# Kernel optimization log

Hardware: AMD Instinct MI355X
Metric: run time of the kernel (lower is better)

## Reference

```python
import jax, jax.numpy as jnp
import numpy as np

BN_EPS = 1e-5


def lstm_scan(x, Wih, Whh, b):
    # x: [B, T, I] -> outputs [B, T, H]; PyTorch gate order i, f, g, o
    B = x.shape[0]
    H = Whh.shape[1]
    xs = jnp.swapaxes(x, 0, 1)  # [T, B, I]

    def step(carry, xt):
        h, c = carry
        z = xt @ Wih.T + h @ Whh.T + b  # [B, 4H]
        i, f, g, o = jnp.split(z, 4, axis=-1)
        c = jax.nn.sigmoid(f) * c + jax.nn.sigmoid(i) * jnp.tanh(g)
        h = jax.nn.sigmoid(o) * jnp.tanh(c)
        return (h, c), h

    init = (jnp.zeros((B, H), x.dtype), jnp.zeros((B, H), x.dtype))
    _, hs = jax.lax.scan(step, init, xs)
    return jnp.swapaxes(hs, 0, 1)


def bilstm(x, Wf, Uf, bf, Wr, Ur, br):
    fwd = lstm_scan(x, Wf, Uf, bf)
    rev = lstm_scan(x[:, ::-1], Wr, Ur, br)[:, ::-1]
    return jnp.concatenate([fwd, rev], axis=-1)


def batchnorm(x, g, b):
    # training-mode BN: batch mean, biased variance (PyTorch forward default)
    mu = x.mean(axis=0)
    var = x.var(axis=0)
    return g * (x - mu) * jax.lax.rsqrt(var + BN_EPS) + b


def setup_inputs() -> dict:
    key = jax.random.key(0)
    ks = jax.random.split(key, 20)
    B = 1048576
    idx = jax.random.randint(ks[0], (B, 1), 0, 8).astype(jnp.float32)
    feats = jax.random.normal(ks[1], (B, 7), dtype=jnp.float32)
    x = jnp.concatenate([idx, feats], axis=1)  # [B, 8]

    def p(k, shape):
        return 0.1 * jax.random.normal(k, shape, dtype=jnp.float32)

    return {
        "x": x,
        "emb": p(ks[2], (8, 2)),
        "W1": p(ks[3], (18, 9)), "b1": p(ks[4], (18,)),
        "g1": jnp.ones((18,), jnp.float32), "be1": jnp.zeros((18,), jnp.float32),
        "W2": p(ks[5], (9, 18)), "b2": p(ks[6], (9,)),
        "g2": jnp.ones((9,), jnp.float32), "be2": jnp.zeros((9,), jnp.float32),
        # lstm1: input 1, hidden 2, bidirectional
        "l1Wf": p(ks[7], (8, 1)), "l1Uf": p(ks[8], (8, 2)), "l1bf": p(ks[9], (8,)),
        "l1Wr": p(ks[10], (8, 1)), "l1Ur": p(ks[11], (8, 2)), "l1br": p(ks[12], (8,)),
        # lstm2: input 4, hidden 1, bidirectional
        "l2Wf": p(ks[13], (4, 4)), "l2Uf": p(ks[14], (4, 1)), "l2bf": p(ks[15], (4,)),
        "l2Wr": p(ks[16], (4, 4)), "l2Ur": p(ks[17], (4, 1)), "l2br": p(ks[18], (4,)),
    }


def reference(x, emb, W1, b1, g1, be1, W2, b2, g2, be2,
              l1Wf, l1Uf, l1bf, l1Wr, l1Ur, l1br,
              l2Wf, l2Uf, l2bf, l2Wr, l2Ur, l2br):
    idx = x[:, 0].astype(jnp.int32)
    e = emb[idx]                                   # [B, 2]
    h = jnp.concatenate([e, x[:, 1:]], axis=1)     # [B, 9]
    h = jax.nn.relu(batchnorm(h @ W1.T + b1, g1, be1))   # [B, 18]
    h = jax.nn.relu(batchnorm(h @ W2.T + b2, g2, be2))   # [B, 9]
    h = h[:, :, None]                              # [B, 9, 1]
    h = jax.nn.relu(bilstm(h, l1Wf, l1Uf, l1bf, l1Wr, l1Ur, l1br))  # [B, 9, 4]
    h = bilstm(h, l2Wf, l2Uf, l2bf, l2Wr, l2Ur, l2br)               # [B, 9, 2]
    return h.reshape(-1, 9, 2)
```

## Files before the change

kernel.cpp:

```cpp
#include <hip/hip_runtime.h>

#define LOG2E 1.4426950408889634f
#define BN_EPS 1e-5f

__device__ __forceinline__ float sigf(float x){
    return __builtin_amdgcn_rcpf(1.f + __builtin_amdgcn_exp2f(-LOG2E * x));
}
__device__ __forceinline__ float tanh_(float x){
    return 1.f - 2.f * __builtin_amdgcn_rcpf(__builtin_amdgcn_exp2f((2.f*LOG2E) * x) + 1.f);
}
__device__ __forceinline__ float relu_(float x){ return fmaxf(x, 0.f); }

__device__ __forceinline__ float wsum(float v){
    #pragma unroll
    for (int m = 32; m >= 1; m >>= 1) v += __shfl_xor(v, m, 64);
    return v;
}

__device__ __forceinline__ void z1_row(const float* __restrict__ x, const float* __restrict__ emb,
                                       const float* __restrict__ W1, const float* __restrict__ b1,
                                       long row, float z1[18])
{
    const float4* xv = (const float4*)(x + row * 8);
    float4 p = xv[0];
    float4 q = xv[1];
    int idx = (int)p.x;
    float2 e = ((const float2*)emb)[idx];
    float h0[9];
    h0[0] = e.x; h0[1] = e.y;
    h0[2] = p.y; h0[3] = p.z; h0[4] = p.w;
    h0[5] = q.x; h0[6] = q.y; h0[7] = q.z; h0[8] = q.w;
    #pragma unroll
    for (int k = 0; k < 18; ++k){
        float s = b1[k];
        #pragma unroll
        for (int j = 0; j < 9; ++j) s = fmaf(W1[k*9 + j], h0[j], s);
        z1[k] = s;
    }
}

__global__ __launch_bounds__(256) void k_stats1(const float* __restrict__ x, const float* __restrict__ emb,
                                                const float* __restrict__ W1, const float* __restrict__ b1,
                                                float* __restrict__ stats, int B)
{
    float as[18], aq[18];
    #pragma unroll
    for (int k = 0; k < 18; ++k){ as[k] = 0.f; aq[k] = 0.f; }
    long base = (long)blockIdx.x * 1024 + threadIdx.x;
    #pragma unroll
    for (int r = 0; r < 4; ++r){
        long row = base + r * 256;
        if (row < B){
            float z1[18];
            z1_row(x, emb, W1, b1, row, z1);
            #pragma unroll
            for (int k = 0; k < 18; ++k){ as[k] += z1[k]; aq[k] = fmaf(z1[k], z1[k], aq[k]); }
        }
    }
    __shared__ float sm[36];
    if (threadIdx.x < 36) sm[threadIdx.x] = 0.f;
    __syncthreads();
    bool l0 = (threadIdx.x & 63) == 0;
    #pragma unroll
    for (int k = 0; k < 18; ++k){
        float s = wsum(as[k]);
        float q = wsum(aq[k]);
        if (l0){ atomicAdd(&sm[k], s); atomicAdd(&sm[18 + k], q); }
    }
    __syncthreads();
    if (threadIdx.x < 36) atomicAdd(&stats[threadIdx.x], sm[threadIdx.x]);
}

__global__ __launch_bounds__(256) void k_stats2(const float* __restrict__ x, const float* __restrict__ emb,
                                                const float* __restrict__ W1, const float* __restrict__ b1,
                                                const float* __restrict__ g1, const float* __restrict__ be1,
                                                const float* __restrict__ W2, const float* __restrict__ b2,
                                                float* __restrict__ stats, int B)
{
    float invB = 1.f / (float)B;
    float sc[18], sh[18];
    #pragma unroll
    for (int k = 0; k < 18; ++k){
        float mu  = stats[k] * invB;
        float var = fmaf(-mu, mu, stats[18 + k] * invB);
        float rs  = __builtin_amdgcn_rsqf(var + BN_EPS);
        sc[k] = g1[k] * rs;
        sh[k] = fmaf(-mu, sc[k], be1[k]);
    }
    float as[9], aq[9];
    #pragma unroll
    for (int k = 0; k < 9; ++k){ as[k] = 0.f; aq[k] = 0.f; }
    long base = (long)blockIdx.x * 1024 + threadIdx.x;
    #pragma unroll
    for (int r = 0; r < 4; ++r){
        long row = base + r * 256;
        if (row < B){
            float z1[18];
            z1_row(x, emb, W1, b1, row, z1);
            float a1[18];
            #pragma unroll
            for (int k = 0; k < 18; ++k) a1[k] = relu_(fmaf(sc[k], z1[k], sh[k]));
            #pragma unroll
            for (int k = 0; k < 9; ++k){
                float s = b2[k];
                #pragma unroll
                for (int j = 0; j < 18; ++j) s = fmaf(W2[k*18 + j], a1[j], s);
                as[k] += s; aq[k] = fmaf(s, s, aq[k]);
            }
        }
    }
    __shared__ float sm[18];
    if (threadIdx.x < 18) sm[threadIdx.x] = 0.f;
    __syncthreads();
    bool l0 = (threadIdx.x & 63) == 0;
    #pragma unroll
    for (int k = 0; k < 9; ++k){
        float s = wsum(as[k]);
        float q = wsum(aq[k]);
        if (l0){ atomicAdd(&sm[k], s); atomicAdd(&sm[9 + k], q); }
    }
    __syncthreads();
    if (threadIdx.x < 18) atomicAdd(&stats[36 + threadIdx.x], sm[threadIdx.x]);
}

template<bool REV>
__device__ __forceinline__ void lstm1(const float* __restrict__ W, const float* __restrict__ U,
                                      const float* __restrict__ bb, const float xin[9], float out[9][2])
{
    float h[2] = {0.f, 0.f}, c[2] = {0.f, 0.f};
    #pragma unroll
    for (int s = 0; s < 9; ++s){
        const int t = REV ? 8 - s : s;
        float xt = xin[t];
        float z[8];
        #pragma unroll
        for (int r = 0; r < 8; ++r)
            z[r] = fmaf(W[r], xt, fmaf(U[2*r], h[0], fmaf(U[2*r + 1], h[1], bb[r])));
        #pragma unroll
        for (int k = 0; k < 2; ++k){
            float ig = sigf(z[k]);
            float fg = sigf(z[2 + k]);
            float gg = tanh_(z[4 + k]);
            float og = sigf(z[6 + k]);
            c[k] = fmaf(fg, c[k], ig * gg);
            h[k] = og * tanh_(c[k]);
        }
        out[t][0] = h[0]; out[t][1] = h[1];
    }
}

template<bool REV>
__device__ __forceinline__ void lstm2(const float* __restrict__ W, const float* __restrict__ U,
                                      const float* __restrict__ bb, const float uin[9][4], float out[9])
{
    float h = 0.f, c = 0.f;
    #pragma unroll
    for (int s = 0; s < 9; ++s){
        const int t = REV ? 8 - s : s;
        float z[4];
        #pragma unroll
        for (int r = 0; r < 4; ++r){
            float acc = fmaf(U[r], h, bb[r]);
            #pragma unroll
            for (int j = 0; j < 4; ++j) acc = fmaf(W[4*r + j], uin[t][j], acc);
            z[r] = acc;
        }
        float ig = sigf(z[0]);
        float fg = sigf(z[1]);
        float gg = tanh_(z[2]);
        float og = sigf(z[3]);
        c = fmaf(fg, c, ig * gg);
        h = og * tanh_(c);
        out[t] = h;
    }
}

__global__ __launch_bounds__(256) void k_main(const float* __restrict__ x, const float* __restrict__ emb,
    const float* __restrict__ W1, const float* __restrict__ b1,
    const float* __restrict__ g1, const float* __restrict__ be1,
    const float* __restrict__ W2, const float* __restrict__ b2,
    const float* __restrict__ g2, const float* __restrict__ be2,
    const float* __restrict__ w1f, const float* __restrict__ u1f, const float* __restrict__ c1f,
    const float* __restrict__ w1r, const float* __restrict__ u1r, const float* __restrict__ c1r,
    const float* __restrict__ w2f, const float* __restrict__ u2f, const float* __restrict__ c2f,
    const float* __restrict__ w2r, const float* __restrict__ u2r, const float* __restrict__ c2r,
    const float* __restrict__ stats, float* __restrict__ out, int B)
{
    long row = (long)blockIdx.x * 256 + threadIdx.x;
    if (row >= B) return;
    float invB = 1.f / (float)B;

    float z1[18];
    z1_row(x, emb, W1, b1, row, z1);
    float a1[18];
    #pragma unroll
    for (int k = 0; k < 18; ++k){
        float mu  = stats[k] * invB;
        float var = fmaf(-mu, mu, stats[18 + k] * invB);
        float rs  = __builtin_amdgcn_rsqf(var + BN_EPS);
        a1[k] = relu_(fmaf(g1[k] * rs, z1[k] - mu, be1[k]));
    }
    float a2[9];
    #pragma unroll
    for (int k = 0; k < 9; ++k){
        float s = b2[k];
        #pragma unroll
        for (int j = 0; j < 18; ++j) s = fmaf(W2[k*18 + j], a1[j], s);
        float mu  = stats[36 + k] * invB;
        float var = fmaf(-mu, mu, stats[45 + k] * invB);
        float rs  = __builtin_amdgcn_rsqf(var + BN_EPS);
        a2[k] = relu_(fmaf(g2[k] * rs, s - mu, be2[k]));
    }

    float hf[9][2], hr[9][2];
    lstm1<false>(w1f, u1f, c1f, a2, hf);
    lstm1<true >(w1r, u1r, c1r, a2, hr);

    float u[9][4];
    #pragma unroll
    for (int t = 0; t < 9; ++t){
        u[t][0] = relu_(hf[t][0]);
        u[t][1] = relu_(hf[t][1]);
        u[t][2] = relu_(hr[t][0]);
        u[t][3] = relu_(hr[t][1]);
    }

    float of[9], orr[9];
    lstm2<false>(w2f, u2f, c2f, u, of);
    lstm2<true >(w2r, u2r, c2r, u, orr);

    float2* op = (float2*)(out + row * 18);
    #pragma unroll
    for (int t = 0; t < 9; ++t) op[t] = make_float2(of[t], orr[t]);
}

extern "C" void kernel_launch(void* const* d_in, const int* in_sizes, int n_in,
                              void* d_out, int out_size, void* d_ws, size_t ws_size,
                              hipStream_t stream)
{
    const float* x    = (const float*)d_in[0];
    const float* emb  = (const float*)d_in[1];
    const float* W1   = (const float*)d_in[2];
    const float* b1   = (const float*)d_in[3];
    const float* g1   = (const float*)d_in[4];
    const float* be1  = (const float*)d_in[5];
    const float* W2   = (const float*)d_in[6];
    const float* b2   = (const float*)d_in[7];
    const float* g2   = (const float*)d_in[8];
    const float* be2  = (const float*)d_in[9];
    const float* l1Wf = (const float*)d_in[10];
    const float* l1Uf = (const float*)d_in[11];
    const float* l1bf = (const float*)d_in[12];
    const float* l1Wr = (const float*)d_in[13];
    const float* l1Ur = (const float*)d_in[14];
    const float* l1br = (const float*)d_in[15];
    const float* l2Wf = (const float*)d_in[16];
    const float* l2Uf = (const float*)d_in[17];
    const float* l2bf = (const float*)d_in[18];
    const float* l2Wr = (const float*)d_in[19];
    const float* l2Ur = (const float*)d_in[20];
    const float* l2br = (const float*)d_in[21];

    int B = in_sizes[0] / 8;
    float* stats = (float*)d_ws;

    hipMemsetAsync(d_ws, 0, 64 * sizeof(float), stream);

    int nb12 = (B + 1023) / 1024;
    int nb3  = (B + 255) / 256;

    k_stats1<<<nb12, 256, 0, stream>>>(x, emb, W1, b1, stats, B);
    k_stats2<<<nb12, 256, 0, stream>>>(x, emb, W1, b1, g1, be1, W2, b2, stats, B);
    k_main<<<nb3, 256, 0, stream>>>(x, emb, W1, b1, g1, be1, W2, b2, g2, be2,
                                    l1Wf, l1Uf, l1bf, l1Wr, l1Ur, l1br,
                                    l2Wf, l2Uf, l2bf, l2Wr, l2Ur, l2br,
                                    stats, (float*)d_out, B);
}
```

Before: 163.1 us.

## Compute BN1 stats from input moments, cache z2, vectorize fused LSTM gates

The first stats pass now accumulates first and second moments of the 9-wide input, and the layer-1 BN mean and variance are derived from these with W1 per block. This removes the 18-wide matmul from that pass. When the workspace is large enough, the second stats pass stores the pre-BN layer-2 activations so the main kernel skips recomputing layer 1 and 2 and reads 36 B/row instead. The forward and reverse LSTM directions run together in packed float vectors, and sigmoid*tanh is fused into a single reciprocal. The risks are the extra global write and read traffic for z2 and some numerical drift in the moment-based variance.

```diff
diff --git a/kernel.cpp b/kernel.cpp
--- a/kernel.cpp
+++ b/kernel.cpp
@@ -3,11 +3,18 @@
 #define LOG2E 1.4426950408889634f
 #define BN_EPS 1e-5f
 
+typedef float f32x2 __attribute__((ext_vector_type(2)));
+typedef float f32x4 __attribute__((ext_vector_type(4)));
+
 __device__ __forceinline__ float sigf(float x){
     return __builtin_amdgcn_rcpf(1.f + __builtin_amdgcn_exp2f(-LOG2E * x));
 }
-__device__ __forceinline__ float tanh_(float x){
-    return 1.f - 2.f * __builtin_amdgcn_rcpf(__builtin_amdgcn_exp2f((2.f*LOG2E) * x) + 1.f);
+__device__ __forceinline__ float sigtanh(float a, float b){
+    float A  = __builtin_amdgcn_exp2f(LOG2E * a);
+    float Bv = __builtin_amdgcn_exp2f((2.f * LOG2E) * b);
+    float num = A * (Bv - 1.f);
+    float den = (1.f + A) * (1.f + Bv);
+    return num * __builtin_amdgcn_rcpf(den);
 }
 __device__ __forceinline__ float relu_(float x){ return fmaxf(x, 0.f); }
 
@@ -17,95 +24,134 @@
     return v;
 }
 
-__device__ __forceinline__ void z1_row(const float* __restrict__ x, const float* __restrict__ emb,
-                                       const float* __restrict__ W1, const float* __restrict__ b1,
-                                       long row, float z1[18])
+__device__ constexpr int TRI(int j, int l){ return j*9 - j*(j-1)/2 + (l - j); }
+
+__device__ __forceinline__ void load_h0(const float* __restrict__ x, const float* __restrict__ emb,
+                                        long row, float h0[9])
 {
     const float4* xv = (const float4*)(x + row * 8);
     float4 p = xv[0];
     float4 q = xv[1];
     int idx = (int)p.x;
     float2 e = ((const float2*)emb)[idx];
-    float h0[9];
     h0[0] = e.x; h0[1] = e.y;
     h0[2] = p.y; h0[3] = p.z; h0[4] = p.w;
     h0[5] = q.x; h0[6] = q.y; h0[7] = q.z; h0[8] = q.w;
-    #pragma unroll
-    for (int k = 0; k < 18; ++k){
-        float s = b1[k];
-        #pragma unroll
-        for (int j = 0; j < 9; ++j) s = fmaf(W1[k*9 + j], h0[j], s);
-        z1[k] = s;
-    }
-}
-
-__global__ __launch_bounds__(256) void k_stats1(const float* __restrict__ x, const float* __restrict__ emb,
-                                                const float* __restrict__ W1, const float* __restrict__ b1,
-                                                float* __restrict__ stats, int B)
-{
-    float as[18], aq[18];
-    #pragma unroll
-    for (int k = 0; k < 18; ++k){ as[k] = 0.f; aq[k] = 0.f; }
+}
+
+__global__ __launch_bounds__(256) void k_moments(const float* __restrict__ x, const float* __restrict__ emb,
+                                                 float* __restrict__ stats, int B)
+{
+    float s9[9], mt[45];
+    #pragma unroll
+    for (int j = 0; j < 9; ++j) s9[j] = 0.f;
+    #pragma unroll
+    for (int t = 0; t < 45; ++t) mt[t] = 0.f;
+
     long base = (long)blockIdx.x * 1024 + threadIdx.x;
     #pragma unroll
     for (int r = 0; r < 4; ++r){
         long row = base + r * 256;
         if (row < B){
-            float z1[18];
-            z1_row(x, emb, W1, b1, row, z1);
-            #pragma unroll
-            for (int k = 0; k < 18; ++k){ as[k] += z1[k]; aq[k] = fmaf(z1[k], z1[k], aq[k]); }
-        }
-    }
-    __shared__ float sm[36];
-    if (threadIdx.x < 36) sm[threadIdx.x] = 0.f;
+            float h0[9];
+            load_h0(x, emb, row, h0);
+            #pragma unroll
+            for (int j = 0; j < 9; ++j){
+                s9[j] += h0[j];
+                #pragma unroll
+                for (int l = j; l < 9; ++l)
+                    mt[TRI(j,l)] = fmaf(h0[j], h0[l], mt[TRI(j,l)]);
+            }
+        }
+    }
+    __shared__ float sm[54];
+    if (threadIdx.x < 54) sm[threadIdx.x] = 0.f;
     __syncthreads();
     bool l0 = (threadIdx.x & 63) == 0;
     #pragma unroll
-    for (int k = 0; k < 18; ++k){
-        float s = wsum(as[k]);
-        float q = wsum(aq[k]);
-        if (l0){ atomicAdd(&sm[k], s); atomicAdd(&sm[18 + k], q); }
-    }
-    __syncthreads();
-    if (threadIdx.x < 36) atomicAdd(&stats[threadIdx.x], sm[threadIdx.x]);
-}
-
+    for (int j = 0; j < 9; ++j){
+        float v = wsum(s9[j]);
+        if (l0) atomicAdd(&sm[j], v);
+    }
+    #pragma unroll
+    for (int t = 0; t < 45; ++t){
+        float v = wsum(mt[t]);
+        if (l0) atomicAdd(&sm[9 + t], v);
+    }
+    __syncthreads();
+    if (threadIdx.x < 9)  atomicAdd(&stats[threadIdx.x], sm[threadIdx.x]);
+    else if (threadIdx.x < 54) atomicAdd(&stats[16 + threadIdx.x - 9], sm[threadIdx.x]);
+}
+
+__device__ __forceinline__ void bn1_from_moments(const float* __restrict__ stats,
+                                                 const float* __restrict__ W1, const float* __restrict__ b1,
+                                                 const float* __restrict__ g1, const float* __restrict__ be1,
+                                                 float invB, float* smem_sc, float* smem_sh)
+{
+    if (threadIdx.x < 18){
+        int k = threadIdx.x;
+        float w[9];
+        #pragma unroll
+        for (int j = 0; j < 9; ++j) w[j] = W1[k*9 + j];
+        float dot9 = 0.f, q = 0.f;
+        #pragma unroll
+        for (int j = 0; j < 9; ++j){
+            dot9 = fmaf(w[j], stats[j], dot9);
+            q = fmaf(w[j]*w[j], stats[16 + TRI(j,j)], q);
+            #pragma unroll
+            for (int l = j+1; l < 9; ++l)
+                q = fmaf(2.f*w[j]*w[l], stats[16 + TRI(j,l)], q);
+        }
+        float m1  = dot9 * invB;
+        float var = fmaf(-m1, m1, q * invB);
+        float mu  = m1 + b1[k];
+        float sc  = g1[k] * __builtin_amdgcn_rsqf(var + BN_EPS);
+        smem_sc[k] = sc;
+        smem_sh[k] = fmaf(-mu, sc, be1[k]);
+    }
+    __syncthreads();
+}
+
+template<int STORE_Z2>
 __global__ __launch_bounds__(256) void k_stats2(const float* __restrict__ x, const float* __restrict__ emb,
                                                 const float* __restrict__ W1, const float* __restrict__ b1,
                                                 const float* __restrict__ g1, const float* __restrict__ be1,
                                                 const float* __restrict__ W2, const float* __restrict__ b2,
-                                                float* __restrict__ stats, int B)
-{
-    float invB = 1.f / (float)B;
-    float sc[18], sh[18];
-    #pragma unroll
-    for (int k = 0; k < 18; ++k){
-        float mu  = stats[k] * invB;
-        float var = fmaf(-mu, mu, stats[18 + k] * invB);
-        float rs  = __builtin_amdgcn_rsqf(var + BN_EPS);
-        sc[k] = g1[k] * rs;
-        sh[k] = fmaf(-mu, sc[k], be1[k]);
-    }
+                                                float* __restrict__ stats, float* __restrict__ z2buf, int B)
+{
+    __shared__ float s_sc[18], s_sh[18];
+    bn1_from_moments(stats, W1, b1, g1, be1, 1.f/(float)B, s_sc, s_sh);
+
+    float sc1[18], sh1[18];
+    #pragma unroll
+    for (int k = 0; k < 18; ++k){ sc1[k] = s_sc[k]; sh1[k] = s_sh[k]; }
+
     float as[9], aq[9];
     #pragma unroll
     for (int k = 0; k < 9; ++k){ as[k] = 0.f; aq[k] = 0.f; }
+
     long base = (long)blockIdx.x * 1024 + threadIdx.x;
     #pragma unroll
     for (int r = 0; r < 4; ++r){
         long row = base + r * 256;
         if (row < B){
-            float z1[18];
-            z1_row(x, emb, W1, b1, row, z1);
+            float h0[9];
+            load_h0(x, emb, row, h0);
             float a1[18];
             #pragma unroll
-            for (int k = 0; k < 18; ++k) a1[k] = relu_(fmaf(sc[k], z1[k], sh[k]));
+            for (int k = 0; k < 18; ++k){
+                float s = b1[k];
+                #pragma unroll
+                for (int j = 0; j < 9; ++j) s = fmaf(W1[k*9 + j], h0[j], s);
+                a1[k] = relu_(fmaf(sc1[k], s, sh1[k]));
+            }
             #pragma unroll
             for (int k = 0; k < 9; ++k){
                 float s = b2[k];
                 #pragma unroll
                 for (int j = 0; j < 18; ++j) s = fmaf(W2[k*18 + j], a1[j], s);
                 as[k] += s; aq[k] = fmaf(s, s, aq[k]);
+                if (STORE_Z2) z2buf[(long)k * B + row] = s;
             }
         }
     }
@@ -120,61 +166,14 @@
         if (l0){ atomicAdd(&sm[k], s); atomicAdd(&sm[9 + k], q); }
     }
     __syncthreads();
-    if (threadIdx.x < 18) atomicAdd(&stats[36 + threadIdx.x], sm[threadIdx.x]);
-}
-
-template<bool REV>
-__device__ __forceinline__ void lstm1(const float* __restrict__ W, const float* __restrict__ U,
-                                      const float* __restrict__ bb, const float xin[9], float out[9][2])
-{
-    float h[2] = {0.f, 0.f}, c[2] = {0.f, 0.f};
-    #pragma unroll
-    for (int s = 0; s < 9; ++s){
-        const int t = REV ? 8 - s : s;
-        float xt = xin[t];
-        float z[8];
-        #pragma unroll
-        for (int r = 0; r < 8; ++r)
-            z[r] = fmaf(W[r], xt, fmaf(U[2*r], h[0], fmaf(U[2*r + 1], h[1], bb[r])));
-        #pragma unroll
-        for (int k = 0; k < 2; ++k){
-            float ig = sigf(z[k]);
-            float fg = sigf(z[2 + k]);
-            float gg = tanh_(z[4 + k]);
-            float og = sigf(z[6 + k]);
-            c[k] = fmaf(fg, c[k], ig * gg);
-            h[k] = og * tanh_(c[k]);
-        }
-        out[t][0] = h[0]; out[t][1] = h[1];
-    }
-}
-
-template<bool REV>
-__device__ __forceinline__ void lstm2(const float* __restrict__ W, const float* __restrict__ U,
-                                      const float* __restrict__ bb, const float uin[9][4], float out[9])
-{
-    float h = 0.f, c = 0.f;
-    #pragma unroll
-    for (int s = 0; s < 9; ++s){
-        const int t = REV ? 8 - s : s;
-        float z[4];
-        #pragma unroll
-        for (int r = 0; r < 4; ++r){
-            float acc = fmaf(U[r], h, bb[r]);
-            #pragma unroll
-            for (int j = 0; j < 4; ++j) acc = fmaf(W[4*r + j], uin[t][j], acc);
-            z[r] = acc;
-        }
-        float ig = sigf(z[0]);
-        float fg = sigf(z[1]);
-        float gg = tanh_(z[2]);
-        float og = sigf(z[3]);
-        c = fmaf(fg, c, ig * gg);
-        h = og * tanh_(c);
-        out[t] = h;
-    }
-}
-
+    if (threadIdx.x < 9)       atomicAdd(&stats[64 + threadIdx.x], sm[threadIdx.x]);
+    else if (threadIdx.x < 18) atomicAdd(&stats[80 + threadIdx.x - 9], sm[threadIdx.x]);
+}
+
+__device__ __forceinline__ f32x2 mk2(float a, float b){ f32x2 r; r.x=a; r.y=b; return r; }
+__device__ __forceinline__ f32x4 mk4(float a, float b, float c, float d){ f32x4 r; r.x=a; r.y=b; r.z=c; r.w=d; return r; }
+
+template<int USE_WS>
 __global__ __launch_bounds__(256) void k_main(const float* __restrict__ x, const float* __restrict__ emb,
     const float* __restrict__ W1, const float* __restrict__ b1,
     const float* __restrict__ g1, const float* __restrict__ be1,
@@ -184,54 +183,128 @@
     const float* __restrict__ w1r, const float* __restrict__ u1r, const float* __restrict__ c1r,
     const float* __restrict__ w2f, const float* __restrict__ u2f, const float* __restrict__ c2f,
     const float* __restrict__ w2r, const float* __restrict__ u2r, const float* __restrict__ c2r,
-    const float* __restrict__ stats, float* __restrict__ out, int B)
-{
+    const float* __restrict__ stats, const float* __restrict__ z2buf,
+    float* __restrict__ out, int B)
+{
+    __shared__ float s_sc[18], s_sh[18];
+    float invB = 1.f / (float)B;
+    if (!USE_WS) bn1_from_moments(stats, W1, b1, g1, be1, invB, s_sc, s_sh);
+
     long row = (long)blockIdx.x * 256 + threadIdx.x;
     if (row >= B) return;
-    float invB = 1.f / (float)B;
-
-    float z1[18];
-    z1_row(x, emb, W1, b1, row, z1);
-    float a1[18];
-    #pragma unroll
-    for (int k = 0; k < 18; ++k){
-        float mu  = stats[k] * invB;
-        float var = fmaf(-mu, mu, stats[18 + k] * invB);
-        float rs  = __builtin_amdgcn_rsqf(var + BN_EPS);
-        a1[k] = relu_(fmaf(g1[k] * rs, z1[k] - mu, be1[k]));
-    }
+
     float a2[9];
     #pragma unroll
     for (int k = 0; k < 9; ++k){
-        float s = b2[k];
-        #pragma unroll
-        for (int j = 0; j < 18; ++j) s = fmaf(W2[k*18 + j], a1[j], s);
-        float mu  = stats[36 + k] * invB;
-        float var = fmaf(-mu, mu, stats[45 + k] * invB);
-        float rs  = __builtin_amdgcn_rsqf(var + BN_EPS);
-        a2[k] = relu_(fmaf(g2[k] * rs, s - mu, be2[k]));
-    }
-
-    float hf[9][2], hr[9][2];
-    lstm1<false>(w1f, u1f, c1f, a2, hf);
-    lstm1<true >(w1r, u1r, c1r, a2, hr);
-
-    float u[9][4];
-    #pragma unroll
-    for (int t = 0; t < 9; ++t){
-        u[t][0] = relu_(hf[t][0]);
-        u[t][1] = relu_(hf[t][1]);
-        u[t][2] = relu_(hr[t][0]);
-        u[t][3] = relu_(hr[t][1]);
-    }
-
-    float of[9], orr[9];
-    lstm2<false>(w2f, u2f, c2f, u, of);
-    lstm2<true >(w2r, u2r, c2r, u, orr);
-
-    float2* op = (float2*)(out + row * 18);
-    #pragma unroll
-    for (int t = 0; t < 9; ++t) op[t] = make_float2(of[t], orr[t]);
+        float zc;
+        if (USE_WS){
+            zc = z2buf[(long)k * B + row];
+        } else {
+            zc = 0.f;
+        }
+        a2[k] = zc;
+    }
+    if (!USE_WS){
+        float h0[9];
+        load_h0(x, emb, row, h0);
+        float a1[18];
+        #pragma unroll
+        for (int k = 0; k < 18; ++k){
+            float s = b1[k];
+            #pragma unroll
+            for (int j = 0; j < 9; ++j) s = fmaf(W1[k*9 + j], h0[j], s);
+            a1[k] = relu_(fmaf(s_sc[k], s, s_sh[k]));
+        }
+        #pragma unroll
+        for (int k = 0; k < 9; ++k){
+            float s = b2[k];
+            #pragma unroll
+            for (int j = 0; j < 18; ++j) s = fmaf(W2[k*18 + j], a1[j], s);
+            a2[k] = s;
+        }
+    }
+    #pragma unroll
+    for (int k = 0; k < 9; ++k){
+        float mu  = stats[64 + k] * invB;
+        float var = fmaf(-mu, mu, stats[80 + k] * invB);
+        float sc  = g2[k] * __builtin_amdgcn_rsqf(var + BN_EPS);
+        a2[k] = relu_(fmaf(sc, a2[k] - mu, be2[k]));
+    }
+
+    f32x4 W4[4], U04[4], U14[4], B4[4];
+    #pragma unroll
+    for (int g = 0; g < 4; ++g){
+        W4[g]  = mk4(w1f[2*g], w1f[2*g+1], w1r[2*g], w1r[2*g+1]);
+        U04[g] = mk4(u1f[(2*g)*2], u1f[(2*g+1)*2], u1r[(2*g)*2], u1r[(2*g+1)*2]);
+        U14[g] = mk4(u1f[(2*g)*2+1], u1f[(2*g+1)*2+1], u1r[(2*g)*2+1], u1r[(2*g+1)*2+1]);
+        B4[g]  = mk4(c1f[2*g], c1f[2*g+1], c1r[2*g], c1r[2*g+1]);
+    }
+    f32x4 h4 = {0.f, 0.f, 0.f, 0.f};
+    f32x4 c4 = {0.f, 0.f, 0.f, 0.f};
+    float u_[9][4];
+    #pragma unroll
+    for (int s = 0; s < 9; ++s){
+        const int tf = s, tr = 8 - s;
+        f32x4 xt4 = mk4(a2[tf], a2[tf], a2[tr], a2[tr]);
+        f32x4 hx  = mk4(h4.x, h4.x, h4.z, h4.z);
+        f32x4 hy  = mk4(h4.y, h4.y, h4.w, h4.w);
+        f32x4 z[4];
+        #pragma unroll
+        for (int g = 0; g < 4; ++g)
+            z[g] = __builtin_elementwise_fma(W4[g], xt4,
+                    __builtin_elementwise_fma(U04[g], hx,
+                     __builtin_elementwise_fma(U14[g], hy, B4[g])));
+        f32x4 icg, fs;
+        #pragma unroll
+        for (int c = 0; c < 4; ++c){
+            icg[c] = sigtanh(z[0][c], z[2][c]);
+            fs[c]  = sigf(z[1][c]);
+        }
+        c4 = __builtin_elementwise_fma(fs, c4, icg);
+        #pragma unroll
+        for (int c = 0; c < 4; ++c) h4[c] = sigtanh(z[3][c], c4[c]);
+        u_[tf][0] = relu_(h4.x);
+        u_[tf][1] = relu_(h4.y);
+        u_[tr][2] = relu_(h4.z);
+        u_[tr][3] = relu_(h4.w);
+    }
+
+    f32x2 w2v[4][4], u2v[4], b2v[4];
+    #pragma unroll
+    for (int r = 0; r < 4; ++r){
+        #pragma unroll
+        for (int j = 0; j < 4; ++j) w2v[r][j] = mk2(w2f[4*r + j], w2r[4*r + j]);
+        u2v[r] = mk2(u2f[r], u2r[r]);
+        b2v[r] = mk2(c2f[r], c2r[r]);
+    }
+    f32x2 h2 = {0.f, 0.f};
+    f32x2 cc = {0.f, 0.f};
+    long obase = row * 18;
+    #pragma unroll
+    for (int s = 0; s < 9; ++s){
+        const int tf = s, tr = 8 - s;
+        f32x2 z[4];
+        #pragma unroll
+        for (int r = 0; r < 4; ++r){
+            f32x2 acc = __builtin_elementwise_fma(u2v[r], h2, b2v[r]);
+            #pragma unroll
+            for (int j = 0; j < 4; ++j)
+                acc = __builtin_elementwise_fma(w2v[r][j], mk2(u_[tf][j], u_[tr][j]), acc);
+            z[r] = acc;
+        }
+        f32x2 icg, fs;
+        #pragma unroll
+        for (int c = 0; c < 2; ++c){
+            icg[c] = sigtanh(z[0][c], z[2][c]);
+            fs[c]  = sigf(z[1][c]);
+        }
+        cc = __builtin_elementwise_fma(fs, cc, icg);
+        float hfo = sigtanh(z[3][0], cc.x);
+        float hro = sigtanh(z[3][1], cc.y);
+        h2 = mk2(hfo, hro);
+        out[obase + 2*tf]     = hfo;
+        out[obase + 2*tr + 1] = hro;
+    }
 }
 
 extern "C" void kernel_launch(void* const* d_in, const int* in_sizes, int n_in,
@@ -263,16 +336,27 @@
 
     int B = in_sizes[0] / 8;
     float* stats = (float*)d_ws;
-
-    hipMemsetAsync(d_ws, 0, 64 * sizeof(float), stream);
+    float* z2buf = (float*)d_ws + 1024;
+    size_t need = (1024 + (size_t)9 * B) * sizeof(float);
+    bool use_ws = ws_size >= need;
+
+    hipMemsetAsync(d_ws, 0, 128 * sizeof(float), stream);
 
     int nb12 = (B + 1023) / 1024;
     int nb3  = (B + 255) / 256;
 
-    k_stats1<<<nb12, 256, 0, stream>>>(x, emb, W1, b1, stats, B);
-    k_stats2<<<nb12, 256, 0, stream>>>(x, emb, W1, b1, g1, be1, W2, b2, stats, B);
-    k_main<<<nb3, 256, 0, stream>>>(x, emb, W1, b1, g1, be1, W2, b2, g2, be2,
-                                    l1Wf, l1Uf, l1bf, l1Wr, l1Ur, l1br,
-                                    l2Wf, l2Uf, l2bf, l2Wr, l2Ur, l2br,
-                                    stats, (float*)d_out, B);
-}
+    k_moments<<<nb12, 256, 0, stream>>>(x, emb, stats, B);
+    if (use_ws){
+        k_stats2<1><<<nb12, 256, 0, stream>>>(x, emb, W1, b1, g1, be1, W2, b2, stats, z2buf, B);
+        k_main<1><<<nb3, 256, 0, stream>>>(x, emb, W1, b1, g1, be1, W2, b2, g2, be2,
+                                           l1Wf, l1Uf, l1bf, l1Wr, l1Ur, l1br,
+                                           l2Wf, l2Uf, l2bf, l2Wr, l2Ur, l2br,
+                                           stats, z2buf, (float*)d_out, B);
+    } else {
+        k_stats2<0><<<nb12, 256, 0, stream>>>(x, emb, W1, b1, g1, be1, W2, b2, stats, z2buf, B);
+        k_main<0><<<nb3, 256, 0, stream>>>(x, emb, W1, b1, g1, be1, W2, b2, g2, be2,
+                                           l1Wf, l1Uf, l1bf, l1Wr, l1Ur, l1br,
+                                           l2Wf, l2Uf, l2bf, l2Wr, l2Ur, l2br,
+                                           stats, z2buf, (float*)d_out, B);
+    }
+}
```

Measured after the change: 152.9 us, median of 2. 6.2% less time.
